# Performance work log

Measured on AMD Instinct MI355X. Metric: run time of the kernel, lower is better.

## Reference

```python
import jax, jax.numpy as jnp
import numpy as np
from jax import lax

BN_EPS = 1e-5


def _bn(t, g, b, m, v):
    # eval-mode BatchNorm2d over channel axis 1
    scale = (g / jnp.sqrt(v + BN_EPS))[None, :, None, None]
    return (t - m[None, :, None, None]) * scale + b[None, :, None, None]


def _conv1x1(t, w):
    # w: (out_c, in_c)
    return jnp.einsum('bchw,oc->bohw', t, w)


def setup_inputs() -> dict:
    key = jax.random.key(0)
    ks = jax.random.split(key, 8)
    B, C_in, H, W = 16, 640, 32, 32
    x = jax.random.normal(ks[0], (B, C_in, H, W), dtype=jnp.float32)

    def bn_params(k, c):
        k1, k2, k3, k4 = jax.random.split(k, 4)
        return (jax.random.normal(k1, (c,), jnp.float32) * 0.1 + 1.0,  # gamma
                jax.random.normal(k2, (c,), jnp.float32) * 0.1,        # beta
                jax.random.normal(k3, (c,), jnp.float32) * 0.1,        # running mean
                jax.random.uniform(k4, (c,), jnp.float32) + 0.5)       # running var

    bn1_g, bn1_b, bn1_m, bn1_v = bn_params(ks[1], 640)
    w_in = jax.random.normal(ks[2], (64, 640), jnp.float32) / np.sqrt(640)
    bnin_g, bnin_b, bnin_m, bnin_v = bn_params(ks[3], 64)
    w_emb = jax.random.normal(ks[4], (640, 1664), jnp.float32) / np.sqrt(1664)
    bne_g, bne_b, bne_m, bne_v = bn_params(ks[5], 640)
    w_out = jax.random.normal(ks[6], (640, 640), jnp.float32) / np.sqrt(640)
    bno_g, bno_b, bno_m, bno_v = bn_params(ks[7], 640)

    return dict(x=x,
                bn1_g=bn1_g, bn1_b=bn1_b, bn1_m=bn1_m, bn1_v=bn1_v,
                w_in=w_in, bnin_g=bnin_g, bnin_b=bnin_b, bnin_m=bnin_m, bnin_v=bnin_v,
                w_emb=w_emb, bne_g=bne_g, bne_b=bne_b, bne_m=bne_m, bne_v=bne_v,
                w_out=w_out, bno_g=bno_g, bno_b=bno_b, bno_m=bno_m, bno_v=bno_v)


def reference(x,
              bn1_g, bn1_b, bn1_m, bn1_v,
              w_in, bnin_g, bnin_b, bnin_m, bnin_v,
              w_emb, bne_g, bne_b, bne_m, bne_v,
              w_out, bno_g, bno_b, bno_m, bno_v):
    KH, KW = 5, 5
    x = jax.nn.relu(_bn(x, bn1_g, bn1_b, bn1_m, bn1_v))
    x = jax.nn.relu(_bn(_conv1x1(x, w_in), bnin_g, bnin_b, bnin_m, bnin_v))
    x0 = jax.nn.relu(x)  # second ReLU in original forward (no-op but faithful)
    # F.normalize(x, dim=1, p=2), eps=1e-12 (PyTorch default)
    norm = jnp.sqrt(jnp.sum(x0 * x0, axis=1, keepdims=True))
    identity = x0 / jnp.maximum(norm, 1e-12)
    b, c, h, w = identity.shape
    # unfold: (b, c*KH*KW, h, w), channel-major ordering matches torch Unfold
    patches = lax.conv_general_dilated_patches(
        identity, (KH, KW), (1, 1), ((2, 2), (2, 2)))
    corr = patches.reshape(b, c, KH * KW, h, w) * identity[:, :, None, :, :]
    corr = corr.reshape(b, c * KH * KW, h, w)
    # featureL2Norm: sqrt(sum(x^2, 1) + 1e-6)
    gs = corr / jnp.sqrt(jnp.sum(corr * corr, axis=1, keepdims=True) + 1e-6)
    feat = jnp.concatenate([identity, gs], axis=1)  # (b, 1664, h, w)
    e = jax.nn.relu(_bn(_conv1x1(feat, w_emb), bne_g, bne_b, bne_m, bne_v))
    out = _bn(_conv1x1(e, w_out), bno_g, bno_b, bno_m, bno_v)
    # dropout in eval mode = identity
    return out
```

## Files before the change

### kernel.cpp

```cpp
#include <hip/hip_runtime.h>
#include <math.h>

#define BN_EPS 1e-5f

using short8  = __attribute__((ext_vector_type(8))) short;
using f32x16  = __attribute__((ext_vector_type(16))) float;


__device__ __forceinline__ float bflo(unsigned u) { return __uint_as_float(u << 16); }
__device__ __forceinline__ float bfhi(unsigned u) { return __uint_as_float(u & 0xffff0000u); }

__device__ __forceinline__ unsigned bf16_rne(float f) {
    unsigned u = __float_as_uint(f);
    return (u + 0x7fffu + ((u >> 16) & 1u)) >> 16;
}
__device__ __forceinline__ unsigned pack_bf16(float lo, float hi) {
    return bf16_rne(lo) | (bf16_rne(hi) << 16);
}
__device__ __forceinline__ unsigned pk_hu(float lo, float hi) {
    unsigned a = __float_as_uint(lo) + 0x8000u;
    unsigned b = __float_as_uint(hi) + 0x8000u;
    return __builtin_amdgcn_perm(b, a, 0x07060302u);
}
__device__ __forceinline__ unsigned pmul_fast(unsigned a, unsigned b) {
    return pk_hu(bflo(a) * bflo(b), bfhi(a) * bfhi(b));
}

__global__ __launch_bounds__(256)
void k_prepAll(const float* __restrict__ g1, const float* __restrict__ b1,
               const float* __restrict__ m1, const float* __restrict__ v1,
               const float* __restrict__ w_in,
               const float* __restrict__ gi, const float* __restrict__ bi,
               const float* __restrict__ mi, const float* __restrict__ vi,
               const float* __restrict__ w_emb,
               const float* __restrict__ ge, const float* __restrict__ be,
               const float* __restrict__ me, const float* __restrict__ ve,
               const float* __restrict__ w_out,
               const float* __restrict__ go, const float* __restrict__ bo,
               const float* __restrict__ mo, const float* __restrict__ vo,
               float* __restrict__ s1, float* __restrict__ b1c,
               float* __restrict__ biasI, float* __restrict__ biasE, float* __restrict__ biasO,
               unsigned* __restrict__ wIt, unsigned* __restrict__ wEt, unsigned* __restrict__ wOt)
{
    __shared__ float row[1664];
    const int tid = threadIdx.x;

    if (blockIdx.x < 640) {
        const int oc = blockIdx.x;
#pragma unroll
        for (int it = 0; it < 2; it++) {
            int u = it * 256 + tid;
            if (u < 416)
                ((float4*)row)[u] = ((const float4*)&w_emb[(size_t)oc * 1664])[u];
        }
        __syncthreads();
        if (tid < 208) {
            int kc = tid >> 2, kh = (tid >> 1) & 1, ksub = tid & 1;
            int k0 = kc * 32 + kh * 16 + ksub * 8;
            float sc = ge[oc] * rsqrtf(ve[oc] + BN_EPS);
            float v[8];
#pragma unroll
            for (int j = 0; j < 8; j++) {
                int kgp = k0 + j;
                int orig;
                if (kgp < 64) orig = kgp;
                else { int t = kgp - 64; orig = 64 + (t & 63) * 25 + (t >> 6); }
                v[j] = row[orig] * sc;
            }
            int mt = oc >> 7, mf = (oc >> 5) & 3;
            int idx = (mt * 52 + kc) * 512 + (mf * 2 + kh) * 64 + ksub * 32 + (oc & 31);
            ((uint4*)wEt)[idx] = make_uint4(pack_bf16(v[0], v[1]), pack_bf16(v[2], v[3]),
                                            pack_bf16(v[4], v[5]), pack_bf16(v[6], v[7]));
        }
        return;
    }

    int i = (blockIdx.x - 640) * 256 + tid;

    if (i < 640) {
        float s = g1[i] * rsqrtf(v1[i] + BN_EPS);
        s1[i] = s; b1c[i] = b1[i] - m1[i] * s;
    } else if (i < 704) {
        int c = i - 640;
        float s = gi[c] * rsqrtf(vi[c] + BN_EPS);
        biasI[c] = bi[c] - mi[c] * s;
    } else if (i < 1344) {
        int c = i - 704;
        float s = ge[c] * rsqrtf(ve[c] + BN_EPS);
        biasE[c] = be[c] - me[c] * s;
    } else if (i < 1984) {
        int c = i - 1344;
        float s = go[c] * rsqrtf(vo[c] + BN_EPS);
        biasO[c] = bo[c] - mo[c] * s;
    }

    if (i >= 2048 && i < 7168) {
        int u = i - 2048;
        int kc = u >> 8, w = u & 255;
        int mf = w >> 7, kh = (w >> 6) & 1, sl = w & 63;
        int oc = mf * 32 + (sl & 31);
        int k0 = kc * 32 + kh * 16 + (sl >> 5) * 8;
        float sc = gi[oc] * rsqrtf(vi[oc] + BN_EPS);
        unsigned d[4];
#pragma unroll
        for (int q = 0; q < 4; q++)
            d[q] = pack_bf16(w_in[oc * 640 + k0 + 2 * q] * sc,
                             w_in[oc * 640 + k0 + 2 * q + 1] * sc);
        ((uint4*)wIt)[u] = make_uint4(d[0], d[1], d[2], d[3]);
    }

    if (i >= 8192 && i < 59392) {
        int u = i - 8192;
        int ci = u >> 9, w = u & 511;
        int mt = ci / 20, kc = ci - mt * 20;
        int mf = w >> 7, kh = (w >> 6) & 1, sl = w & 63;
        int oc = mt * 128 + mf * 32 + (sl & 31);
        int k0 = kc * 32 + kh * 16 + (sl >> 5) * 8;
        float sc = go[oc] * rsqrtf(vo[oc] + BN_EPS);
        unsigned d[4];
#pragma unroll
        for (int q = 0; q < 4; q++)
            d[q] = pack_bf16(w_out[oc * 640 + k0 + 2 * q] * sc,
                             w_out[oc * 640 + k0 + 2 * q + 1] * sc);
        ((uint4*)wOt)[u] = make_uint4(d[0], d[1], d[2], d[3]);
    }
}

__device__ __forceinline__ uint4 gen_feat_unit(const short* slab, const short* ctrs,
                                               int kcAbs, int t)
{
    const int hf = t >> 7, sl = t & 63;
    const int bkh = (t >> 6) & 1;
    const int cl = bkh * 16 + (sl >> 5) * 8;
    if (kcAbs < 2) {
        int spxC = (hf + 2) * 36 + (sl & 31) + 2;
        return *(const uint4*)&slab[spxC * 72 + kcAbs * 32 + cl];
    } else {
        int pxl = hf * 32 + (sl & 31);
        int idx = kcAbs - 2;
        int ksp = idx >> 1;
        int cb = (idx & 1) * 32 + cl;
        int kho = ksp / 5, kwo = ksp - kho * 5;
        int spx = (hf + kho) * 36 + (sl & 31) + kwo;
        const unsigned* nb = (const unsigned*)&slab[spx * 72 + cb];
        const unsigned* ct = (const unsigned*)&ctrs[pxl * 72 + cb];
        return make_uint4(pmul_fast(nb[0], ct[0]), pmul_fast(nb[1], ct[1]),
                          pmul_fast(nb[2], ct[2]), pmul_fast(nb[3], ct[3]));
    }
}

__global__ __launch_bounds__(640, 3)
void k_mega(const float* __restrict__ x,
            const float* __restrict__ s1, const float* __restrict__ b1c,
            const unsigned* __restrict__ wIt, const float* __restrict__ biasI,
            const unsigned* __restrict__ wEt, const float* __restrict__ biasE,
            const unsigned* __restrict__ wOt, const float* __restrict__ biasO,
            float* __restrict__ out)
{
    __shared__ __align__(16) char Lds[106112];
    short* slab  = (short*)Lds;
    float* s1L   = (float*)(Lds + 31104);
    float* b1L   = (float*)(Lds + 31104 + 2560);
    short* ctrs  = (short*)(Lds + 31104);
    float* invDs = (float*)(Lds + 40320);
    char*  stg   = Lds + 40576;
    uint4* Ep    = (uint4*)Lds;

    const int tid = threadIdx.x;
    const int l = tid & 63;
    const int w = tid >> 6;
    const int mt = w >> 1, mf0 = (w & 1) * 2;
    const int pt = blockIdx.x;
    const int b = pt >> 4, r0 = (pt & 15) * 2;

    if (tid < 160)       ((float4*)s1L)[tid]       = ((const float4*)s1)[tid];
    else if (tid < 320)  ((float4*)b1L)[tid - 160] = ((const float4*)b1c)[tid - 160];
    __syncthreads();

    if (w < 7) {
        const int spx = w * 32 + (l & 31);
        const int spxc = spx < 216 ? spx : 215;
        const int sr = spxc / 36, sc = spxc - sr * 36;
        const int r = r0 + sr - 2, cc = sc - 2;
        const bool valid = (spx < 216) && (r >= 0) && (r < 32) && (cc >= 0) && (cc < 32);
        const int rcl = min(max(r, 0), 31), ccl = min(max(cc, 0), 31);
        const float* xp = x + (size_t)b * 655360 + (size_t)(rcl * 32 + ccl);
        const int co = (l >> 5) * 8;

        f32x16 accI[2];
#pragma unroll
        for (int i = 0; i < 2; i++)
#pragma unroll
            for (int rr = 0; rr < 16; rr++) accI[i][rr] = 0.f;

        float xv[16], xn[16];
        uint4 av[2][2], avn[2][2];
#pragma unroll
        for (int kh = 0; kh < 2; kh++)
#pragma unroll
            for (int j = 0; j < 8; j++)
                xv[kh * 8 + j] = xp[(size_t)(kh * 16 + co + j) * 1024];
#pragma unroll
        for (int mi2 = 0; mi2 < 2; mi2++)
#pragma unroll
            for (int kh = 0; kh < 2; kh++)
                av[mi2][kh] = ((const uint4*)wIt)[(mi2 << 7) + (kh << 6) + l];

        for (int kc = 0; kc < 20; kc++) {
            if (kc < 19) {
#pragma unroll
                for (int kh = 0; kh < 2; kh++)
#pragma unroll
                    for (int j = 0; j < 8; j++)
                        xn[kh * 8 + j] = xp[(size_t)((kc + 1) * 32 + kh * 16 + co + j) * 1024];
#pragma unroll
                for (int mi2 = 0; mi2 < 2; mi2++)
#pragma unroll
                    for (int kh = 0; kh < 2; kh++)
                        avn[mi2][kh] = ((const uint4*)wIt)[(kc + 1) * 256 + (mi2 << 7) + (kh << 6) + l];
            }
#pragma unroll
            for (int kh = 0; kh < 2; kh++) {
                const int ch0 = kc * 32 + kh * 16 + co;
                float4 sA = *(const float4*)&s1L[ch0], sB = *(const float4*)&s1L[ch0 + 4];
                float4 bA = *(const float4*)&b1L[ch0], bB = *(const float4*)&b1L[ch0 + 4];
                float vv[8];
                vv[0] = fmaxf(fmaf(xv[kh * 8 + 0], sA.x, bA.x), 0.f);
                vv[1] = fmaxf(fmaf(xv[kh * 8 + 1], sA.y, bA.y), 0.f);
                vv[2] = fmaxf(fmaf(xv[kh * 8 + 2], sA.z, bA.z), 0.f);
                vv[3] = fmaxf(fmaf(xv[kh * 8 + 3], sA.w, bA.w), 0.f);
                vv[4] = fmaxf(fmaf(xv[kh * 8 + 4], sB.x, bB.x), 0.f);
                vv[5] = fmaxf(fmaf(xv[kh * 8 + 5], sB.y, bB.y), 0.f);
                vv[6] = fmaxf(fmaf(xv[kh * 8 + 6], sB.z, bB.z), 0.f);
                vv[7] = fmaxf(fmaf(xv[kh * 8 + 7], sB.w, bB.w), 0.f);
                unsigned bu[4] = { pack_bf16(vv[0], vv[1]), pack_bf16(vv[2], vv[3]),
                                   pack_bf16(vv[4], vv[5]), pack_bf16(vv[6], vv[7]) };
                short8 bf = *(short8*)bu;
                accI[0] = __builtin_amdgcn_mfma_f32_32x32x16_bf16(*(short8*)&av[0][kh], bf, accI[0], 0, 0, 0);
                accI[1] = __builtin_amdgcn_mfma_f32_32x32x16_bf16(*(short8*)&av[1][kh], bf, accI[1], 0, 0, 0);
            }
            if (kc < 19) {
#pragma unroll
                for (int q = 0; q < 16; q++) xv[q] = xn[q];
#pragma unroll
                for (int mi2 = 0; mi2 < 2; mi2++)
#pragma unroll
                    for (int kh = 0; kh < 2; kh++) av[mi2][kh] = avn[mi2][kh];
            }
        }
        float ss = 0.f;
#pragma unroll
        for (int mi2 = 0; mi2 < 2; mi2++)
#pragma unroll
            for (int rg = 0; rg < 4; rg++) {
                float4 bb = *(const float4*)&biasI[mi2 * 32 + 8 * rg + 4 * (l >> 5)];
#pragma unroll
                for (int q = 0; q < 4; q++) {
                    float bv = (q == 0) ? bb.x : (q == 1) ? bb.y : (q == 2) ? bb.z : bb.w;
                    float t = fmaxf(accI[mi2][rg * 4 + q] + bv, 0.f);
                    accI[mi2][rg * 4 + q] = t;
                    ss = fmaf(t, t, ss);
                }
            }
        ss += __shfl_xor(ss, 32);
        float inv = 1.f / fmaxf(sqrtf(ss), 1e-12f);
        if (spx < 216) {
#pragma unroll
            for (int mi2 = 0; mi2 < 2; mi2++)
#pragma unroll
                for (int rg = 0; rg < 4; rg++) {
                    unsigned d0 = pack_bf16(accI[mi2][rg * 4 + 0] * inv, accI[mi2][rg * 4 + 1] * inv);
                    unsigned d1 = pack_bf16(accI[mi2][rg * 4 + 2] * inv, accI[mi2][rg * 4 + 3] * inv);
                    if (!valid) { d0 = 0u; d1 = 0u; }
                    *(uint2*)&slab[spx * 72 + mi2 * 32 + 8 * rg + 4 * (l >> 5)] = make_uint2(d0, d1);
                }
        }
    }
    __syncthreads();

    if (tid < 512) {
        int px = tid >> 3, part = tid & 7;
        int rh = px >> 5, rw = px & 31;
        float ctr[8];
        const unsigned* cp = (const unsigned*)&slab[((rh + 2) * 36 + rw + 2) * 72 + part * 8];
#pragma unroll
        for (int d = 0; d < 4; d++) { ctr[2 * d] = bflo(cp[d]); ctr[2 * d + 1] = bfhi(cp[d]); }
        float sum = 0.f;
#pragma unroll
        for (int k = 0; k < 25; k++) {
            const int kh = k / 5, kw = k % 5;
            const unsigned* nb = (const unsigned*)&slab[((rh + kh) * 36 + rw + kw) * 72 + part * 8];
#pragma unroll
            for (int d = 0; d < 4; d++) {
                float q0 = bflo(nb[d]) * ctr[2 * d];
                float q1 = bfhi(nb[d]) * ctr[2 * d + 1];
                sum = fmaf(q0, q0, sum); sum = fmaf(q1, q1, sum);
            }
        }
        sum += __shfl_xor(sum, 1);
        sum += __shfl_xor(sum, 2);
        sum += __shfl_xor(sum, 4);
        if (part == 0) invDs[px] = rsqrtf(sum + 1e-6f);
    }
    __syncthreads();

    if (tid < 512) {
        int px = tid >> 3, q = tid & 7;
        int spx = ((px >> 5) + 2) * 36 + (px & 31) + 2;
        const unsigned* src = (const unsigned*)&slab[spx * 72 + q * 8];
        float iv = invDs[px];
        unsigned d[4];
#pragma unroll
        for (int dd = 0; dd < 4; dd++)
            d[dd] = pk_hu(bflo(src[dd]) * iv, bfhi(src[dd]) * iv);
        *(uint4*)&ctrs[px * 72 + q * 8] = make_uint4(d[0], d[1], d[2], d[3]);
    }
    __syncthreads();

    const uint4* A = (const uint4*)wEt + (size_t)(mt * 52) * 512;

    f32x16 acc[2][2];
#pragma unroll
    for (int i = 0; i < 2; i++)
#pragma unroll
        for (int j = 0; j < 2; j++)
#pragma unroll
            for (int r = 0; r < 16; r++) acc[i][j][r] = 0.f;

    uint4 avc[2][2];
#pragma unroll
    for (int mi = 0; mi < 2; mi++)
#pragma unroll
        for (int kh = 0; kh < 2; kh++)
            avc[mi][kh] = A[(((mf0 + mi) * 2 + kh) << 6) + l];

#pragma unroll
    for (int k = 0; k < 4; k++) {
        int u = tid + k * 640;
        if (u < 2048) {
            uint4 f = gen_feat_unit(slab, ctrs, (u >> 8), u & 255);
            *(uint4*)&stg[u * 16] = f;
        }
    }
    __syncthreads();

    uint4 bvc[2][2];
#pragma unroll
    for (int ni = 0; ni < 2; ni++)
#pragma unroll
        for (int kh = 0; kh < 2; kh++)
            bvc[ni][kh] = *(const uint4*)&stg[((ni << 7) + (kh << 6) + l) * 16];

#pragma unroll 1
    for (int c = 0; c < 6; c++) {
        const int cur = c & 1, nxt = cur ^ 1;
        const int base = c * 8;
        {
            const int nunits = (c < 5) ? 2048 : 1024;
            const int nbase = base + 8;
#pragma unroll
            for (int k = 0; k < 4; k++) {
                int u = tid + k * 640;
                if (u < nunits) {
                    uint4 f = gen_feat_unit(slab, ctrs, nbase + (u >> 8), u & 255);
                    *(uint4*)&stg[nxt * 32768 + u * 16] = f;
                }
            }
        }
#pragma unroll
        for (int kcL = 0; kcL < 8; kcL++) {
            const int kc = base + kcL;
            uint4 avn[2][2];
#pragma unroll
            for (int mi = 0; mi < 2; mi++)
#pragma unroll
                for (int kh = 0; kh < 2; kh++)
                    avn[mi][kh] = A[(size_t)(kc + 1) * 512 + (((mf0 + mi) * 2 + kh) << 6) + l];
            uint4 bvn[2][2];
            if (kcL < 7) {
#pragma unroll
                for (int ni = 0; ni < 2; ni++)
#pragma unroll
                    for (int kh = 0; kh < 2; kh++)
                        bvn[ni][kh] = *(const uint4*)&stg[cur * 32768 + ((kcL + 1) * 256 + (ni << 7) + (kh << 6) + l) * 16];
            }
#pragma unroll
            for (int kh = 0; kh < 2; kh++) {
                acc[0][0] = __builtin_amdgcn_mfma_f32_32x32x16_bf16(*(short8*)&avc[0][kh], *(short8*)&bvc[0][kh], acc[0][0], 0, 0, 0);
                acc[0][1] = __builtin_amdgcn_mfma_f32_32x32x16_bf16(*(short8*)&avc[0][kh], *(short8*)&bvc[1][kh], acc[0][1], 0, 0, 0);
                acc[1][0] = __builtin_amdgcn_mfma_f32_32x32x16_bf16(*(short8*)&avc[1][kh], *(short8*)&bvc[0][kh], acc[1][0], 0, 0, 0);
                acc[1][1] = __builtin_amdgcn_mfma_f32_32x32x16_bf16(*(short8*)&avc[1][kh], *(short8*)&bvc[1][kh], acc[1][1], 0, 0, 0);
            }
#pragma unroll
            for (int mi = 0; mi < 2; mi++)
#pragma unroll
                for (int kh = 0; kh < 2; kh++) avc[mi][kh] = avn[mi][kh];
            if (kcL < 7) {
#pragma unroll
                for (int ni = 0; ni < 2; ni++)
#pragma unroll
                    for (int kh = 0; kh < 2; kh++) bvc[ni][kh] = bvn[ni][kh];
            }
        }
        __syncthreads();
#pragma unroll
        for (int ni = 0; ni < 2; ni++)
#pragma unroll
            for (int kh = 0; kh < 2; kh++)
                bvc[ni][kh] = *(const uint4*)&stg[nxt * 32768 + ((ni << 7) + (kh << 6) + l) * 16];
    }
#pragma unroll
    for (int kcL = 0; kcL < 4; kcL++) {
        const int kc = 48 + kcL;
        uint4 avn[2][2], bvn[2][2];
        if (kcL < 3) {
#pragma unroll
            for (int mi = 0; mi < 2; mi++)
#pragma unroll
                for (int kh = 0; kh < 2; kh++)
                    avn[mi][kh] = A[(size_t)(kc + 1) * 512 + (((mf0 + mi) * 2 + kh) << 6) + l];
#pragma unroll
            for (int ni = 0; ni < 2; ni++)
#pragma unroll
                for (int kh = 0; kh < 2; kh++)
                    bvn[ni][kh] = *(const uint4*)&stg[((kcL + 1) * 256 + (ni << 7) + (kh << 6) + l) * 16];
        }
#pragma unroll
        for (int kh = 0; kh < 2; kh++) {
            acc[0][0] = __builtin_amdgcn_mfma_f32_32x32x16_bf16(*(short8*)&avc[0][kh], *(short8*)&bvc[0][kh], acc[0][0], 0, 0, 0);
            acc[0][1] = __builtin_amdgcn_mfma_f32_32x32x16_bf16(*(short8*)&avc[0][kh], *(short8*)&bvc[1][kh], acc[0][1], 0, 0, 0);
            acc[1][0] = __builtin_amdgcn_mfma_f32_32x32x16_bf16(*(short8*)&avc[1][kh], *(short8*)&bvc[0][kh], acc[1][0], 0, 0, 0);
            acc[1][1] = __builtin_amdgcn_mfma_f32_32x32x16_bf16(*(short8*)&avc[1][kh], *(short8*)&bvc[1][kh], acc[1][1], 0, 0, 0);
        }
        if (kcL < 3) {
#pragma unroll
            for (int mi = 0; mi < 2; mi++)
#pragma unroll
                for (int kh = 0; kh < 2; kh++) avc[mi][kh] = avn[mi][kh];
#pragma unroll
            for (int ni = 0; ni < 2; ni++)
#pragma unroll
                for (int kh = 0; kh < 2; kh++) bvc[ni][kh] = bvn[ni][kh];
        }
    }
    __syncthreads();

#pragma unroll
    for (int mi = 0; mi < 2; mi++) {
        const int kbase = (w * 2 + mi) * 256;
#pragma unroll
        for (int ni = 0; ni < 2; ni++) {
#pragma unroll
            for (int rg = 0; rg < 4; rg++) {
                int ocb = w * 64 + mi * 32 + 8 * rg + 4 * (l >> 5);
                float4 bb = *(const float4*)&biasE[ocb];
                unsigned d0 = pack_bf16(fmaxf(acc[mi][ni][rg * 4 + 0] + bb.x, 0.f),
                                        fmaxf(acc[mi][ni][rg * 4 + 1] + bb.y, 0.f));
                unsigned d1 = pack_bf16(fmaxf(acc[mi][ni][rg * 4 + 2] + bb.z, 0.f),
                                        fmaxf(acc[mi][ni][rg * 4 + 3] + bb.w, 0.f));
                int unit = kbase + (ni << 7) + ((rg >> 1) << 6) + ((rg & 1) << 5) + (l & 31);
                ((uint2*)Ep)[unit * 2 + (l >> 5)] = make_uint2(d0, d1);
            }
        }
    }
    __syncthreads();

    const int p0 = pt * 64;
    const int hw0 = p0 & 1023;
    const uint4* Ao = (const uint4*)wOt + (size_t)(mt * 20) * 512;

    f32x16 acc2[2][2];
#pragma unroll
    for (int i = 0; i < 2; i++)
#pragma unroll
        for (int j = 0; j < 2; j++)
#pragma unroll
            for (int r = 0; r < 16; r++) acc2[i][j][r] = 0.f;

    uint4 aoc[2][2], boc[2][2];
#pragma unroll
    for (int mi = 0; mi < 2; mi++)
#pragma unroll
        for (int kh = 0; kh < 2; kh++)
            aoc[mi][kh] = Ao[(((mf0 + mi) * 2 + kh) << 6) + l];
#pragma unroll
    for (int ni = 0; ni < 2; ni++)
#pragma unroll
        for (int kh = 0; kh < 2; kh++)
            boc[ni][kh] = Ep[(ni << 7) + (kh << 6) + l];

#pragma unroll 4
    for (int kc = 0; kc < 20; kc++) {
        uint4 aon[2][2], bon[2][2];
        if (kc < 19) {
#pragma unroll
            for (int mi = 0; mi < 2; mi++)
#pragma unroll
                for (int kh = 0; kh < 2; kh++)
                    aon[mi][kh] = Ao[(size_t)(kc + 1) * 512 + (((mf0 + mi) * 2 + kh) << 6) + l];
#pragma unroll
            for (int ni = 0; ni < 2; ni++)
#pragma unroll
                for (int kh = 0; kh < 2; kh++)
                    bon[ni][kh] = Ep[(kc + 1) * 256 + (ni << 7) + (kh << 6) + l];
        }
#pragma unroll
        for (int kh = 0; kh < 2; kh++) {
            acc2[0][0] = __builtin_amdgcn_mfma_f32_32x32x16_bf16(*(short8*)&aoc[0][kh], *(short8*)&boc[0][kh], acc2[0][0], 0, 0, 0);
            acc2[0][1] = __builtin_amdgcn_mfma_f32_32x32x16_bf16(*(short8*)&aoc[0][kh], *(short8*)&boc[1][kh], acc2[0][1], 0, 0, 0);
            acc2[1][0] = __builtin_amdgcn_mfma_f32_32x32x16_bf16(*(short8*)&aoc[1][kh], *(short8*)&boc[0][kh], acc2[1][0], 0, 0, 0);
            acc2[1][1] = __builtin_amdgcn_mfma_f32_32x32x16_bf16(*(short8*)&aoc[1][kh], *(short8*)&boc[1][kh], acc2[1][1], 0, 0, 0);
        }
        if (kc < 19) {
#pragma unroll
            for (int mi = 0; mi < 2; mi++)
#pragma unroll
                for (int kh = 0; kh < 2; kh++) aoc[mi][kh] = aon[mi][kh];
#pragma unroll
            for (int ni = 0; ni < 2; ni++)
#pragma unroll
                for (int kh = 0; kh < 2; kh++) boc[ni][kh] = bon[ni][kh];
        }
    }

#pragma unroll
    for (int mi = 0; mi < 2; mi++)
#pragma unroll
        for (int ni = 0; ni < 2; ni++) {
            int pxl = ni * 32 + (l & 31);
#pragma unroll
            for (int r = 0; r < 16; r++) {
                int oc = w * 64 + mi * 32 + (r & 3) + 8 * (r >> 2) + 4 * (l >> 5);
                out[((size_t)b * 640 + oc) * 1024 + hw0 + pxl] = acc2[mi][ni][r] + biasO[oc];
            }
        }
}

extern "C" void kernel_launch(void* const* d_in, const int* in_sizes, int n_in,
                              void* d_out, int out_size, void* d_ws, size_t ws_size,
                              hipStream_t stream)
{
    const float* x    = (const float*)d_in[0];
    const float* g1   = (const float*)d_in[1];
    const float* b1   = (const float*)d_in[2];
    const float* m1   = (const float*)d_in[3];
    const float* v1   = (const float*)d_in[4];
    const float* w_in = (const float*)d_in[5];
    const float* gi   = (const float*)d_in[6];
    const float* bi   = (const float*)d_in[7];
    const float* mi   = (const float*)d_in[8];
    const float* vi   = (const float*)d_in[9];
    const float* w_emb= (const float*)d_in[10];
    const float* ge   = (const float*)d_in[11];
    const float* be   = (const float*)d_in[12];
    const float* me   = (const float*)d_in[13];
    const float* ve   = (const float*)d_in[14];
    const float* w_out= (const float*)d_in[15];
    const float* go   = (const float*)d_in[16];
    const float* bo   = (const float*)d_in[17];
    const float* mo   = (const float*)d_in[18];
    const float* vo   = (const float*)d_in[19];

    char* ws = (char*)d_ws;
    float*    s1    = (float*)(ws + 0);
    float*    b1c   = (float*)(ws + 2560);
    float*    biasI = (float*)(ws + 5120);
    float*    biasE = (float*)(ws + 5376);
    float*    biasO = (float*)(ws + 7936);
    unsigned* wIt   = (unsigned*)(ws + 16384);
    unsigned* wOt   = (unsigned*)(ws + 98304);
    unsigned* wEt   = (unsigned*)(ws + 917504);
    float*    out   = (float*)d_out;

    k_prepAll<<<872, 256, 0, stream>>>(g1, b1, m1, v1, w_in, gi, bi, mi, vi,
                                       w_emb, ge, be, me, ve, w_out, go, bo, mo, vo,
                                       s1, b1c, biasI, biasE, biasO, wIt, wEt, wOt);
    k_mega<<<256, 640, 0, stream>>>(x, s1, b1c, wIt, biasI,
                                    wEt, biasE, wOt, biasO, out);
}
```

Before: 194.0 us.

## Precompute BN1+ReLU bf16-packed input in prep kernel for vector loads

```diff
diff --git a/kernel.cpp b/kernel.cpp
--- a/kernel.cpp
+++ b/kernel.cpp
@@ -27,7 +27,8 @@
 }
 
 __global__ __launch_bounds__(256)
-void k_prepAll(const float* __restrict__ g1, const float* __restrict__ b1,
+void k_prepAll(const float* __restrict__ x,
+               const float* __restrict__ g1, const float* __restrict__ b1,
                const float* __restrict__ m1, const float* __restrict__ v1,
                const float* __restrict__ w_in,
                const float* __restrict__ gi, const float* __restrict__ bi,
@@ -38,12 +39,39 @@
                const float* __restrict__ w_out,
                const float* __restrict__ go, const float* __restrict__ bo,
                const float* __restrict__ mo, const float* __restrict__ vo,
-               float* __restrict__ s1, float* __restrict__ b1c,
                float* __restrict__ biasI, float* __restrict__ biasE, float* __restrict__ biasO,
-               unsigned* __restrict__ wIt, unsigned* __restrict__ wEt, unsigned* __restrict__ wOt)
+               unsigned* __restrict__ wIt, unsigned* __restrict__ wEt, unsigned* __restrict__ wOt,
+               unsigned* __restrict__ xpk)
 {
     __shared__ float row[1664];
     const int tid = threadIdx.x;
+
+    if (blockIdx.x >= 872) {
+        const int id2 = blockIdx.x - 872;
+        const int b = id2 / 20, kc = id2 - b * 20;
+#pragma unroll 4
+        for (int it = 0; it < 16; it++) {
+            const int co8 = it >> 2;
+            const int p = (it & 3) * 256 + tid;
+            const int ch0 = kc * 32 + co8 * 8;
+            unsigned d[4];
+#pragma unroll
+            for (int q = 0; q < 4; q++) {
+                float v[2];
+#pragma unroll
+                for (int h = 0; h < 2; h++) {
+                    int ch = ch0 + 2 * q + h;
+                    float sc = g1[ch] * rsqrtf(v1[ch] + BN_EPS);
+                    float bc = b1[ch] - m1[ch] * sc;
+                    v[h] = fmaxf(fmaf(x[((size_t)b * 640 + ch) * 1024 + p], sc, bc), 0.f);
+                }
+                d[q] = pack_bf16(v[0], v[1]);
+            }
+            *(uint4*)((char*)xpk + (((size_t)(b * 20 + kc) * 1024 + p) * 64 + co8 * 16)) =
+                make_uint4(d[0], d[1], d[2], d[3]);
+        }
+        return;
+    }
 
     if (blockIdx.x < 640) {
         const int oc = blockIdx.x;
@@ -77,18 +105,15 @@
 
     int i = (blockIdx.x - 640) * 256 + tid;
 
-    if (i < 640) {
-        float s = g1[i] * rsqrtf(v1[i] + BN_EPS);
-        s1[i] = s; b1c[i] = b1[i] - m1[i] * s;
-    } else if (i < 704) {
-        int c = i - 640;
+    if (i < 64) {
+        int c = i;
         float s = gi[c] * rsqrtf(vi[c] + BN_EPS);
         biasI[c] = bi[c] - mi[c] * s;
-    } else if (i < 1344) {
+    } else if (i >= 704 && i < 1344) {
         int c = i - 704;
         float s = ge[c] * rsqrtf(ve[c] + BN_EPS);
         biasE[c] = be[c] - me[c] * s;
-    } else if (i < 1984) {
+    } else if (i >= 1344 && i < 1984) {
         int c = i - 1344;
         float s = go[c] * rsqrtf(vo[c] + BN_EPS);
         biasO[c] = bo[c] - mo[c] * s;
@@ -150,8 +175,7 @@
 }
 
 __global__ __launch_bounds__(640, 3)
-void k_mega(const float* __restrict__ x,
-            const float* __restrict__ s1, const float* __restrict__ b1c,
+void k_mega(const unsigned* __restrict__ xpk,
             const unsigned* __restrict__ wIt, const float* __restrict__ biasI,
             const unsigned* __restrict__ wEt, const float* __restrict__ biasE,
             const unsigned* __restrict__ wOt, const float* __restrict__ biasO,
@@ -159,8 +183,6 @@
 {
     __shared__ __align__(16) char Lds[106112];
     short* slab  = (short*)Lds;
-    float* s1L   = (float*)(Lds + 31104);
-    float* b1L   = (float*)(Lds + 31104 + 2560);
     short* ctrs  = (short*)(Lds + 31104);
     float* invDs = (float*)(Lds + 40320);
     char*  stg   = Lds + 40576;
@@ -172,10 +194,6 @@
     const int mt = w >> 1, mf0 = (w & 1) * 2;
     const int pt = blockIdx.x;
     const int b = pt >> 4, r0 = (pt & 15) * 2;
-
-    if (tid < 160)       ((float4*)s1L)[tid]       = ((const float4*)s1)[tid];
-    else if (tid < 320)  ((float4*)b1L)[tid - 160] = ((const float4*)b1c)[tid - 160];
-    __syncthreads();
 
     if (w < 7) {
         const int spx = w * 32 + (l & 31);
@@ -184,8 +202,8 @@
         const int r = r0 + sr - 2, cc = sc - 2;
         const bool valid = (spx < 216) && (r >= 0) && (r < 32) && (cc >= 0) && (cc < 32);
         const int rcl = min(max(r, 0), 31), ccl = min(max(cc, 0), 31);
-        const float* xp = x + (size_t)b * 655360 + (size_t)(rcl * 32 + ccl);
-        const int co = (l >> 5) * 8;
+        const int pcl = rcl * 32 + ccl;
+        const char* xb = (const char*)xpk + ((size_t)b * 1310720 + (size_t)pcl * 64 + ((l >> 5) * 16));
 
         f32x16 accI[2];
 #pragma unroll
@@ -193,13 +211,10 @@
 #pragma unroll
             for (int rr = 0; rr < 16; rr++) accI[i][rr] = 0.f;
 
-        float xv[16], xn[16];
-        uint4 av[2][2], avn[2][2];
+        uint4 bq[2], bqn[2], av[2][2], avn[2][2];
 #pragma unroll
         for (int kh = 0; kh < 2; kh++)
-#pragma unroll
-            for (int j = 0; j < 8; j++)
-                xv[kh * 8 + j] = xp[(size_t)(kh * 16 + co + j) * 1024];
+            bq[kh] = *(const uint4*)(xb + kh * 32);
 #pragma unroll
         for (int mi2 = 0; mi2 < 2; mi2++)
 #pragma unroll
@@ -210,9 +225,7 @@
             if (kc < 19) {
 #pragma unroll
                 for (int kh = 0; kh < 2; kh++)
-#pragma unroll
-                    for (int j = 0; j < 8; j++)
-                        xn[kh * 8 + j] = xp[(size_t)((kc + 1) * 32 + kh * 16 + co + j) * 1024];
+                    bqn[kh] = *(const uint4*)(xb + (size_t)(kc + 1) * 65536 + kh * 32);
 #pragma unroll
                 for (int mi2 = 0; mi2 < 2; mi2++)
 #pragma unroll
@@ -221,27 +234,12 @@
             }
 #pragma unroll
             for (int kh = 0; kh < 2; kh++) {
-                const int ch0 = kc * 32 + kh * 16 + co;
-                float4 sA = *(const float4*)&s1L[ch0], sB = *(const float4*)&s1L[ch0 + 4];
-                float4 bA = *(const float4*)&b1L[ch0], bB = *(const float4*)&b1L[ch0 + 4];
-                float vv[8];
-                vv[0] = fmaxf(fmaf(xv[kh * 8 + 0], sA.x, bA.x), 0.f);
-                vv[1] = fmaxf(fmaf(xv[kh * 8 + 1], sA.y, bA.y), 0.f);
-                vv[2] = fmaxf(fmaf(xv[kh * 8 + 2], sA.z, bA.z), 0.f);
-                vv[3] = fmaxf(fmaf(xv[kh * 8 + 3], sA.w, bA.w), 0.f);
-                vv[4] = fmaxf(fmaf(xv[kh * 8 + 4], sB.x, bB.x), 0.f);
-                vv[5] = fmaxf(fmaf(xv[kh * 8 + 5], sB.y, bB.y), 0.f);
-                vv[6] = fmaxf(fmaf(xv[kh * 8 + 6], sB.z, bB.z), 0.f);
-                vv[7] = fmaxf(fmaf(xv[kh * 8 + 7], sB.w, bB.w), 0.f);
-                unsigned bu[4] = { pack_bf16(vv[0], vv[1]), pack_bf16(vv[2], vv[3]),
-                                   pack_bf16(vv[4], vv[5]), pack_bf16(vv[6], vv[7]) };
-                short8 bf = *(short8*)bu;
-                accI[0] = __builtin_amdgcn_mfma_f32_32x32x16_bf16(*(short8*)&av[0][kh], bf, accI[0], 0, 0, 0);
-                accI[1] = __builtin_amdgcn_mfma_f32_32x32x16_bf16(*(short8*)&av[1][kh], bf, accI[1], 0, 0, 0);
+                accI[0] = __builtin_amdgcn_mfma_f32_32x32x16_bf16(*(short8*)&av[0][kh], *(short8*)&bq[kh], accI[0], 0, 0, 0);
+                accI[1] = __builtin_amdgcn_mfma_f32_32x32x16_bf16(*(short8*)&av[1][kh], *(short8*)&bq[kh], accI[1], 0, 0, 0);
             }
             if (kc < 19) {
 #pragma unroll
-                for (int q = 0; q < 16; q++) xv[q] = xn[q];
+                for (int kh = 0; kh < 2; kh++) bq[kh] = bqn[kh];
 #pragma unroll
                 for (int mi2 = 0; mi2 < 2; mi2++)
 #pragma unroll
@@ -562,19 +560,18 @@
     const float* vo   = (const float*)d_in[19];
 
     char* ws = (char*)d_ws;
-    float*    s1    = (float*)(ws + 0);
-    float*    b1c   = (float*)(ws + 2560);
     float*    biasI = (float*)(ws + 5120);
     float*    biasE = (float*)(ws + 5376);
     float*    biasO = (float*)(ws + 7936);
     unsigned* wIt   = (unsigned*)(ws + 16384);
     unsigned* wOt   = (unsigned*)(ws + 98304);
     unsigned* wEt   = (unsigned*)(ws + 917504);
+    unsigned* xpk   = (unsigned*)(ws + 3047424);
     float*    out   = (float*)d_out;
 
-    k_prepAll<<<872, 256, 0, stream>>>(g1, b1, m1, v1, w_in, gi, bi, mi, vi,
-                                       w_emb, ge, be, me, ve, w_out, go, bo, mo, vo,
-                                       s1, b1c, biasI, biasE, biasO, wIt, wEt, wOt);
-    k_mega<<<256, 640, 0, stream>>>(x, s1, b1c, wIt, biasI,
+    k_prepAll<<<1192, 256, 0, stream>>>(x, g1, b1, m1, v1, w_in, gi, bi, mi, vi,
+                                        w_emb, ge, be, me, ve, w_out, go, bo, mo, vo,
+                                        biasI, biasE, biasO, wIt, wEt, wOt, xpk);
+    k_mega<<<256, 640, 0, stream>>>(xpk, wIt, biasI,
                                     wEt, biasE, wOt, biasO, out);
 }
```

After: 202.7 us. 4.5% more time.
